# Kernel tuning notes

Measured on AMD Instinct MI355X. Metric: run time of the kernel, lower is better.

Reference implementation:

```python
import jax, jax.numpy as jnp
import numpy as np

HEADS = 16
KV_HEADS = 4
HEAD_DIM = 64
EMBED = 1024


def setup_inputs() -> dict:
    key = jax.random.key(0)
    k1, k2, k3, k4, k5 = jax.random.split(key, 5)
    B, S, G, E = 1, 2048, 2, EMBED
    scale = 1.0 / np.sqrt(E)
    x = jax.random.normal(k1, (B, S, G, E), dtype=jnp.float32)
    Wq = jax.random.normal(k2, (E, HEADS * HEAD_DIM), dtype=jnp.float32) * scale
    Wk = jax.random.normal(k3, (E, KV_HEADS * HEAD_DIM), dtype=jnp.float32) * scale
    Wv = jax.random.normal(k4, (E, KV_HEADS * HEAD_DIM), dtype=jnp.float32) * scale
    Wo = jax.random.normal(k5, (E, E), dtype=jnp.float32) * scale
    return {"x": x, "Wq": Wq, "Wk": Wk, "Wv": Wv, "Wo": Wo}


def reference(x, Wq, Wk, Wv, Wo):
    B, S, G, E = x.shape
    ratio = HEADS // KV_HEADS
    # projections over last dim (no bias, no activation)
    q = (x @ Wq).reshape(B, S, G, HEADS, HEAD_DIM)
    k = (x @ Wk).reshape(B, S, G, KV_HEADS, HEAD_DIM)
    v = (x @ Wv).reshape(B, S, G, KV_HEADS, HEAD_DIM)
    # GQA repeat_kv: each kv head repeated `ratio` times consecutively
    k = jnp.repeat(k, ratio, axis=3)  # [B,S,G,H,D]
    v = jnp.repeat(v, ratio, axis=3)
    # energy: [B,G,H,Q,K]
    energy = jnp.einsum('bqghd,bkghd->bghqk', q, k)
    # causal mask: triu(1) set to -inf (before the sqrt scaling, as in source)
    causal = jnp.triu(jnp.ones((S, S), dtype=bool), 1)
    energy = jnp.where(causal, -jnp.inf, energy)
    scores = jax.nn.softmax(energy / np.sqrt(HEAD_DIM), axis=-1)
    attn = jnp.einsum('bghqv,bvghd->bqghd', scores, v)
    attn = attn.reshape(B, S, G, E)
    return attn @ Wo
```

## Files before the change

kernel.cpp:

```cpp
#include <hip/hip_runtime.h>
#include <cstdint>
#include <cstddef>

typedef __bf16 bf16_t;
typedef bf16_t bf16x8 __attribute__((ext_vector_type(8)));
typedef float f32x4 __attribute__((ext_vector_type(4)));

__device__ inline bf16x8 load8(const float* p) {
  f32x4 a = *reinterpret_cast<const f32x4*>(p);
  f32x4 b = *reinterpret_cast<const f32x4*>(p + 4);
  bf16x8 r;
  r[0] = (bf16_t)a[0]; r[1] = (bf16_t)a[1];
  r[2] = (bf16_t)a[2]; r[3] = (bf16_t)a[3];
  r[4] = (bf16_t)b[0]; r[5] = (bf16_t)b[1];
  r[6] = (bf16_t)b[2]; r[7] = (bf16_t)b[3];
  return r;
}
__device__ inline bf16x8 load8(const bf16_t* p) {
  return *reinterpret_cast<const bf16x8*>(p);
}

__global__ __launch_bounds__(256) void cvt1_k(
    const float* __restrict__ x, const float* __restrict__ Wq,
    const float* __restrict__ Wk, const float* __restrict__ Wv,
    bf16_t* __restrict__ xb, bf16_t* __restrict__ wqb,
    bf16_t* __restrict__ wkb, bf16_t* __restrict__ wvb) {
  const int b = blockIdx.x;
  const float* s;
  bf16_t* d;
  size_t off;
  if (b < 2048) { s = x; d = xb; off = (size_t)b * 2048; }
  else if (b < 2560) { s = Wq; d = wqb; off = (size_t)(b - 2048) * 2048; }
  else if (b < 2688) { s = Wk; d = wkb; off = (size_t)(b - 2560) * 2048; }
  else { s = Wv; d = wvb; off = (size_t)(b - 2688) * 2048; }
  const size_t i = off + (size_t)threadIdx.x * 8;
  *reinterpret_cast<bf16x8*>(d + i) = load8(s + i);
}

__global__ __launch_bounds__(256) void cvt2_k(const float* __restrict__ Wo,
                                              bf16_t* __restrict__ wob) {
  const size_t i = (size_t)blockIdx.x * 2048 + (size_t)threadIdx.x * 8;
  *reinterpret_cast<bf16x8*>(wob + i) = load8(Wo + i);
}

template <typename OutT>
__device__ inline void gemm128_body(const bf16_t* __restrict__ A,
                                    const bf16_t* __restrict__ B,
                                    OutT* __restrict__ C, int m0, int K,
                                    int BN, int bn0, int CN, int cn0,
                                    float alpha) {
  __shared__ __align__(16) bf16_t As[128][40];
  __shared__ __align__(16) bf16_t Bs[128][40];

  const int tid = threadIdx.x;
  const int wave = tid >> 6, lane = tid & 63;
  const int quad = lane >> 4, l16 = lane & 15;
  const int moff = (wave & 1) * 64, noff = (wave >> 1) * 64;

  f32x4 acc[4][4];
#pragma unroll
  for (int mt = 0; mt < 4; ++mt)
#pragma unroll
    for (int nt = 0; nt < 4; ++nt) acc[mt][nt] = {0.f, 0.f, 0.f, 0.f};

  const int arow = tid >> 1, ak0 = (tid & 1) * 16;
  const int bkr = tid & 31, bnc = (tid >> 5) * 16;

  bf16x8 a0, a1, b0, b1;
  {
    const bf16_t* ap = &A[(size_t)(m0 + arow) * K + ak0];
    a0 = load8(ap); a1 = load8(ap + 8);
    const bf16_t* bp = &B[(size_t)bkr * BN + bn0 + bnc];
    b0 = load8(bp); b1 = load8(bp + 8);
  }

  for (int k0 = 0; k0 < K; k0 += 32) {
    *reinterpret_cast<bf16x8*>(&As[arow][ak0]) = a0;
    *reinterpret_cast<bf16x8*>(&As[arow][ak0 + 8]) = a1;
#pragma unroll
    for (int j = 0; j < 8; ++j) {
      Bs[bnc + j][bkr] = b0[j];
      Bs[bnc + 8 + j][bkr] = b1[j];
    }
    __syncthreads();
    if (k0 + 32 < K) {
      const bf16_t* ap = &A[(size_t)(m0 + arow) * K + k0 + 32 + ak0];
      a0 = load8(ap); a1 = load8(ap + 8);
      const bf16_t* bp = &B[(size_t)(k0 + 32 + bkr) * BN + bn0 + bnc];
      b0 = load8(bp); b1 = load8(bp + 8);
    }
    bf16x8 af[4], bfr[4];
#pragma unroll
    for (int mt = 0; mt < 4; ++mt)
      af[mt] =
          *reinterpret_cast<const bf16x8*>(&As[moff + mt * 16 + l16][quad * 8]);
#pragma unroll
    for (int nt = 0; nt < 4; ++nt)
      bfr[nt] =
          *reinterpret_cast<const bf16x8*>(&Bs[noff + nt * 16 + l16][quad * 8]);
#pragma unroll
    for (int mt = 0; mt < 4; ++mt)
#pragma unroll
      for (int nt = 0; nt < 4; ++nt)
        acc[mt][nt] = __builtin_amdgcn_mfma_f32_16x16x32_bf16(
            af[mt], bfr[nt], acc[mt][nt], 0, 0, 0);
    __syncthreads();
  }

#pragma unroll
  for (int mt = 0; mt < 4; ++mt) {
    const int crow = m0 + moff + mt * 16 + quad * 4;
#pragma unroll
    for (int nt = 0; nt < 4; ++nt) {
      const int ccol = cn0 + noff + nt * 16 + l16;
#pragma unroll
      for (int r = 0; r < 4; ++r)
        C[(size_t)(crow + r) * CN + ccol] = (OutT)(acc[mt][nt][r] * alpha);
    }
  }
}

__global__ __launch_bounds__(256, 3) void qkv_k(
    const bf16_t* __restrict__ x, const bf16_t* __restrict__ Wq,
    const bf16_t* __restrict__ Wk, const bf16_t* __restrict__ Wv,
    bf16_t* __restrict__ Qo, bf16_t* __restrict__ Ko, bf16_t* __restrict__ Vo) {
  const int n0 = blockIdx.x * 128;
  const int m0 = blockIdx.y * 128;
  const bf16_t* B;
  bf16_t* C;
  int BN, bn0;
  float alpha;
  if (n0 < 1024) {
    B = Wq; C = Qo; BN = 1024; bn0 = n0; alpha = 0.125f;
  } else if (n0 < 1280) {
    B = Wk; C = Ko; BN = 256; bn0 = n0 - 1024; alpha = 1.0f;
  } else {
    B = Wv; C = Vo; BN = 256; bn0 = n0 - 1280; alpha = 1.0f;
  }
  gemm128_body<bf16_t>(x, B, C, m0, 1024, BN, bn0, BN, bn0, alpha);
}

template <typename OutT>
__global__ __launch_bounds__(256, 3) void gemm128_k(
    const bf16_t* __restrict__ A, const bf16_t* __restrict__ B,
    OutT* __restrict__ C, int K, int N, float alpha) {
  gemm128_body<OutT>(A, B, C, blockIdx.y * 128, K, N, blockIdx.x * 128, N,
                     blockIdx.x * 128, alpha);
}

__global__ __launch_bounds__(256) void transpose_v_k(
    const bf16_t* __restrict__ V, bf16_t* __restrict__ VT) {
  __shared__ bf16_t Vs[64][72];
  const int tid = threadIdx.x;
  const int kt0 = blockIdx.x * 64;
  const int ghk = blockIdx.y;
  const int g = ghk >> 2, kh = ghk & 3;
#pragma unroll
  for (int i = 0; i < 2; ++i) {
    const int c = tid + 256 * i;
    const int row = c >> 3, d0 = (c & 7) * 8;
    *reinterpret_cast<bf16x8*>(&Vs[row][d0]) = *reinterpret_cast<const bf16x8*>(
        &V[((size_t)(kt0 + row) * 2 + g) * 256 + kh * 64 + d0]);
  }
  __syncthreads();
#pragma unroll
  for (int i = 0; i < 2; ++i) {
    const int c = tid + 256 * i;
    const int d = c >> 3, k0 = (c & 7) * 8;
    bf16x8 v;
#pragma unroll
    for (int j = 0; j < 8; ++j) v[j] = Vs[k0 + j][d];
    *reinterpret_cast<bf16x8*>(&VT[((size_t)ghk * 64 + d) * 2048 + kt0 + k0]) =
        v;
  }
}

__global__ __launch_bounds__(128, 2) void flash5_k(
    const bf16_t* __restrict__ Q, const bf16_t* __restrict__ K,
    const bf16_t* __restrict__ VT, bf16_t* __restrict__ ATTN) {
  __shared__ __align__(16) bf16_t Ks[64][64];
  __shared__ __align__(16) bf16_t Vs[64][64];
  __shared__ __align__(16) bf16_t Ps[2][32][64];

  const int tid = threadIdx.x;
  const int w = tid >> 6, lane = tid & 63;
  const int quad = lane >> 4, l16 = lane & 15;
  const int b = blockIdx.x;
  const int T = (b & 1) ? (31 - (b >> 1)) : (b >> 1);
  const int gh = blockIdx.y;
  const int g = gh >> 4, h = gh & 15, kh = h >> 2;
  const int qbase = T * 64 + w * 32;
  const int swz = ((l16 >> 2) & 3) << 4;
  const int rsw = l16 & 7;

  bf16x8 qf[2][2];
#pragma unroll
  for (int rg = 0; rg < 2; ++rg)
#pragma unroll
    for (int t = 0; t < 2; ++t)
      qf[rg][t] = *reinterpret_cast<const bf16x8*>(
          &Q[((size_t)(qbase + rg * 16 + l16) * 2 + g) * 1024 + h * 64 +
             t * 32 + quad * 8]);

  f32x4 O[2][4];
  f32x4 lp[2];
#pragma unroll
  for (int rg = 0; rg < 2; ++rg) {
    lp[rg] = {0.f, 0.f, 0.f, 0.f};
#pragma unroll
    for (int d = 0; d < 4; ++d) O[rg][d] = {0.f, 0.f, 0.f, 0.f};
  }

  bf16x8 kr[4], vr[4];
#pragma unroll
  for (int i = 0; i < 4; ++i) {
    const int c = tid + 128 * i;
    const int row = c >> 3, e0 = (c & 7) * 8;
    kr[i] = *reinterpret_cast<const bf16x8*>(
        &K[((size_t)(row)*2 + g) * 256 + kh * 64 + e0]);
    vr[i] = *reinterpret_cast<const bf16x8*>(
        &VT[((size_t)(g * 4 + kh) * 64 + row) * 2048 + e0]);
  }

  for (int kt = 0; kt <= T; ++kt) {
#pragma unroll
    for (int i = 0; i < 4; ++i) {
      const int c = tid + 128 * i;
      const int row = c >> 3;
      const int pb = (((c & 7) ^ (row & 7)) << 3);
      *reinterpret_cast<bf16x8*>(&Ks[row][pb]) = kr[i];
      *reinterpret_cast<bf16x8*>(&Vs[row][pb]) = vr[i];
    }
    __syncthreads();
    if (kt < T) {
      const int nt0 = (kt + 1) * 64;
#pragma unroll
      for (int i = 0; i < 4; ++i) {
        const int c = tid + 128 * i;
        const int row = c >> 3, e0 = (c & 7) * 8;
        kr[i] = *reinterpret_cast<const bf16x8*>(
            &K[((size_t)(nt0 + row) * 2 + g) * 256 + kh * 64 + e0]);
        vr[i] = *reinterpret_cast<const bf16x8*>(
            &VT[((size_t)(g * 4 + kh) * 64 + row) * 2048 + nt0 + e0]);
      }
    }

    f32x4 s[2][4];
#pragma unroll
    for (int nt = 0; nt < 4; ++nt) {
      bf16x8 kf0 = *reinterpret_cast<const bf16x8*>(
          &Ks[nt * 16 + l16][(quad ^ rsw) << 3]);
      bf16x8 kf1 = *reinterpret_cast<const bf16x8*>(
          &Ks[nt * 16 + l16][((4 + quad) ^ rsw) << 3]);
#pragma unroll
      for (int rg = 0; rg < 2; ++rg) {
        f32x4 z = {0.f, 0.f, 0.f, 0.f};
        z = __builtin_amdgcn_mfma_f32_16x16x32_bf16(qf[rg][0], kf0, z, 0, 0, 0);
        s[rg][nt] =
            __builtin_amdgcn_mfma_f32_16x16x32_bf16(qf[rg][1], kf1, z, 0, 0, 0);
      }
    }
    const bool diag = (kt == T);
#pragma unroll
    for (int rg = 0; rg < 2; ++rg) {
#pragma unroll
      for (int nt = 0; nt < 4; ++nt) {
        const int key = nt * 16 + l16;
#pragma unroll
        for (int r = 0; r < 4; ++r) {
          float p = __expf(s[rg][nt][r]);
          if (diag && key > w * 32 + rg * 16 + quad * 4 + r) p = 0.f;
          lp[rg][r] += p;
          Ps[w][rg * 16 + quad * 4 + r][((nt ^ quad) << 4) + l16] = (bf16_t)p;
        }
      }
    }
    bf16x8 pf[2][2];
#pragma unroll
    for (int rg = 0; rg < 2; ++rg)
#pragma unroll
      for (int t = 0; t < 2; ++t)
        pf[rg][t] = *reinterpret_cast<const bf16x8*>(
            &Ps[w][rg * 16 + l16][(t * 32 + quad * 8) ^ swz]);
#pragma unroll
    for (int dnt = 0; dnt < 4; ++dnt) {
      bf16x8 vf0 = *reinterpret_cast<const bf16x8*>(
          &Vs[dnt * 16 + l16][(quad ^ rsw) << 3]);
      bf16x8 vf1 = *reinterpret_cast<const bf16x8*>(
          &Vs[dnt * 16 + l16][((4 + quad) ^ rsw) << 3]);
#pragma unroll
      for (int rg = 0; rg < 2; ++rg) {
        O[rg][dnt] = __builtin_amdgcn_mfma_f32_16x16x32_bf16(
            pf[rg][0], vf0, O[rg][dnt], 0, 0, 0);
        O[rg][dnt] = __builtin_amdgcn_mfma_f32_16x16x32_bf16(
            pf[rg][1], vf1, O[rg][dnt], 0, 0, 0);
      }
    }
    __syncthreads();
  }

#pragma unroll
  for (int rg = 0; rg < 2; ++rg) {
#pragma unroll
    for (int off = 1; off < 16; off <<= 1)
#pragma unroll
      for (int r = 0; r < 4; ++r) lp[rg][r] += __shfl_xor(lp[rg][r], off, 64);
#pragma unroll
    for (int r = 0; r < 4; ++r) {
      const float inv = 1.f / lp[rg][r];
      const int row = qbase + rg * 16 + quad * 4 + r;
#pragma unroll
      for (int dnt = 0; dnt < 4; ++dnt)
        ATTN[((size_t)row * 2 + g) * 1024 + h * 64 + dnt * 16 + l16] =
            (bf16_t)(O[rg][dnt][r] * inv);
    }
  }
}

extern "C" void kernel_launch(void* const* d_in, const int* in_sizes, int n_in,
                              void* d_out, int out_size, void* d_ws,
                              size_t ws_size, hipStream_t stream) {
  (void)in_sizes;
  (void)n_in;
  (void)out_size;
  (void)ws_size;

  const float* x = (const float*)d_in[0];
  const float* Wq = (const float*)d_in[1];
  const float* Wk = (const float*)d_in[2];
  const float* Wv = (const float*)d_in[3];
  const float* Wo = (const float*)d_in[4];
  float* out = (float*)d_out;

  const size_t MB = 1024 * 1024;
  char* ob = (char*)d_out;
  bf16_t* Qtmp = (bf16_t*)ob;
  bf16_t* VTws = (bf16_t*)(ob + 8 * MB);
  bf16_t* wqb = (bf16_t*)(ob + 10 * MB);
  bf16_t* wkb = (bf16_t*)(ob + 12 * MB);
  bf16_t* wvb = (bf16_t*)(ob + 12 * MB + 512 * 1024);
  char* wb = (char*)d_ws;
  bf16_t* Kws = (bf16_t*)wb;
  bf16_t* Vws = (bf16_t*)(wb + 2 * MB);
  bf16_t* ATTNws = (bf16_t*)(wb + 4 * MB);
  bf16_t* xb = ATTNws;
  bf16_t* wob = Kws;

  cvt1_k<<<dim3(2816), dim3(256), 0, stream>>>(x, Wq, Wk, Wv, xb, wqb, wkb,
                                               wvb);
  qkv_k<<<dim3(12, 32), dim3(256), 0, stream>>>(xb, wqb, wkb, wvb, Qtmp, Kws,
                                                Vws);
  transpose_v_k<<<dim3(32, 8), dim3(256), 0, stream>>>(Vws, VTws);
  flash5_k<<<dim3(32, 32), dim3(128), 0, stream>>>(Qtmp, Kws, VTws, ATTNws);
  cvt2_k<<<dim3(512), dim3(256), 0, stream>>>(Wo, wob);
  gemm128_k<float><<<dim3(8, 32), dim3(256), 0, stream>>>(ATTNws, wob, out,
                                                          1024, 1024, 1.0f);
}
```

Baseline: 198.8 us.

## Pre-transpose weights to N-major bf16 and reorder flash tile scheduling

Weights are now converted to bf16 and transposed once, in a tiled shared-memory kernel, so the GEMM B-operand loads become contiguous 16-byte rows written to LDS with vector stores instead of scalar transposed stores. The separate Wo conversion is merged into the weight-transpose kernel, and buffers are relocated to fit. The flash kernel's causal tile ordering changes from alternating pairs to groups of eight in a zigzag pattern for load balance. The cost is an extra transpose pass over the weights.

```diff
diff --git a/kernel.cpp b/kernel.cpp
--- a/kernel.cpp
+++ b/kernel.cpp
@@ -20,35 +20,54 @@
   return *reinterpret_cast<const bf16x8*>(p);
 }
 
-__global__ __launch_bounds__(256) void cvt1_k(
-    const float* __restrict__ x, const float* __restrict__ Wq,
-    const float* __restrict__ Wk, const float* __restrict__ Wv,
-    bf16_t* __restrict__ xb, bf16_t* __restrict__ wqb,
-    bf16_t* __restrict__ wkb, bf16_t* __restrict__ wvb) {
+__global__ __launch_bounds__(256) void cvtx_k(const float* __restrict__ x,
+                                              bf16_t* __restrict__ xb) {
+  const size_t i = (size_t)blockIdx.x * 2048 + (size_t)threadIdx.x * 8;
+  *reinterpret_cast<bf16x8*>(xb + i) = load8(x + i);
+}
+
+__global__ __launch_bounds__(256) void cvtT_k(
+    const float* __restrict__ Wq, const float* __restrict__ Wk,
+    const float* __restrict__ Wv, const float* __restrict__ Wo,
+    bf16_t* __restrict__ wqT, bf16_t* __restrict__ wkT,
+    bf16_t* __restrict__ wvT, bf16_t* __restrict__ woT) {
+  __shared__ bf16_t Ts[64][72];
   const int b = blockIdx.x;
-  const float* s;
-  bf16_t* d;
-  size_t off;
-  if (b < 2048) { s = x; d = xb; off = (size_t)b * 2048; }
-  else if (b < 2560) { s = Wq; d = wqb; off = (size_t)(b - 2048) * 2048; }
-  else if (b < 2688) { s = Wk; d = wkb; off = (size_t)(b - 2560) * 2048; }
-  else { s = Wv; d = wvb; off = (size_t)(b - 2688) * 2048; }
-  const size_t i = off + (size_t)threadIdx.x * 8;
-  *reinterpret_cast<bf16x8*>(d + i) = load8(s + i);
-}
-
-__global__ __launch_bounds__(256) void cvt2_k(const float* __restrict__ Wo,
-                                              bf16_t* __restrict__ wob) {
-  const size_t i = (size_t)blockIdx.x * 2048 + (size_t)threadIdx.x * 8;
-  *reinterpret_cast<bf16x8*>(wob + i) = load8(Wo + i);
+  const float* S;
+  bf16_t* D;
+  int N, idx;
+  if (b < 256) { S = Wq; D = wqT; N = 1024; idx = b; }
+  else if (b < 320) { S = Wk; D = wkT; N = 256; idx = b - 256; }
+  else if (b < 384) { S = Wv; D = wvT; N = 256; idx = b - 320; }
+  else { S = Wo; D = woT; N = 1024; idx = b - 384; }
+  const int ntl = (N == 1024) ? 4 : 2;
+  const int kt0 = (idx >> ntl) * 64;
+  const int n0 = (idx & ((1 << ntl) - 1)) * 64;
+  const int tid = threadIdx.x;
+#pragma unroll
+  for (int i = 0; i < 2; ++i) {
+    const int c = tid + 256 * i;
+    const int row = c >> 3, col0 = (c & 7) * 8;
+    *reinterpret_cast<bf16x8*>(&Ts[row][col0]) =
+        load8(&S[(size_t)(kt0 + row) * N + n0 + col0]);
+  }
+  __syncthreads();
+#pragma unroll
+  for (int i = 0; i < 2; ++i) {
+    const int c = tid + 256 * i;
+    const int nrow = c >> 3, k0 = (c & 7) * 8;
+    bf16x8 v;
+#pragma unroll
+    for (int j = 0; j < 8; ++j) v[j] = Ts[k0 + j][nrow];
+    *reinterpret_cast<bf16x8*>(&D[(size_t)(n0 + nrow) * 1024 + kt0 + k0]) = v;
+  }
 }
 
 template <typename OutT>
-__device__ inline void gemm128_body(const bf16_t* __restrict__ A,
-                                    const bf16_t* __restrict__ B,
-                                    OutT* __restrict__ C, int m0, int K,
-                                    int BN, int bn0, int CN, int cn0,
-                                    float alpha) {
+__device__ inline void gemm_bt_body(const bf16_t* __restrict__ A,
+                                    const bf16_t* __restrict__ BT,
+                                    OutT* __restrict__ C, int m0, int bt0,
+                                    int K, int CN, int cn0, float alpha) {
   __shared__ __align__(16) bf16_t As[128][40];
   __shared__ __align__(16) bf16_t Bs[128][40];
 
@@ -64,29 +83,25 @@
     for (int nt = 0; nt < 4; ++nt) acc[mt][nt] = {0.f, 0.f, 0.f, 0.f};
 
   const int arow = tid >> 1, ak0 = (tid & 1) * 16;
-  const int bkr = tid & 31, bnc = (tid >> 5) * 16;
 
   bf16x8 a0, a1, b0, b1;
   {
     const bf16_t* ap = &A[(size_t)(m0 + arow) * K + ak0];
     a0 = load8(ap); a1 = load8(ap + 8);
-    const bf16_t* bp = &B[(size_t)bkr * BN + bn0 + bnc];
+    const bf16_t* bp = &BT[(size_t)(bt0 + arow) * K + ak0];
     b0 = load8(bp); b1 = load8(bp + 8);
   }
 
   for (int k0 = 0; k0 < K; k0 += 32) {
     *reinterpret_cast<bf16x8*>(&As[arow][ak0]) = a0;
     *reinterpret_cast<bf16x8*>(&As[arow][ak0 + 8]) = a1;
-#pragma unroll
-    for (int j = 0; j < 8; ++j) {
-      Bs[bnc + j][bkr] = b0[j];
-      Bs[bnc + 8 + j][bkr] = b1[j];
-    }
+    *reinterpret_cast<bf16x8*>(&Bs[arow][ak0]) = b0;
+    *reinterpret_cast<bf16x8*>(&Bs[arow][ak0 + 8]) = b1;
     __syncthreads();
     if (k0 + 32 < K) {
       const bf16_t* ap = &A[(size_t)(m0 + arow) * K + k0 + 32 + ak0];
       a0 = load8(ap); a1 = load8(ap + 8);
-      const bf16_t* bp = &B[(size_t)(k0 + 32 + bkr) * BN + bn0 + bnc];
+      const bf16_t* bp = &BT[(size_t)(bt0 + arow) * K + k0 + 32 + ak0];
       b0 = load8(bp); b1 = load8(bp + 8);
     }
     bf16x8 af[4], bfr[4];
@@ -121,30 +136,30 @@
 }
 
 __global__ __launch_bounds__(256, 3) void qkv_k(
-    const bf16_t* __restrict__ x, const bf16_t* __restrict__ Wq,
-    const bf16_t* __restrict__ Wk, const bf16_t* __restrict__ Wv,
+    const bf16_t* __restrict__ x, const bf16_t* __restrict__ wqT,
+    const bf16_t* __restrict__ wkT, const bf16_t* __restrict__ wvT,
     bf16_t* __restrict__ Qo, bf16_t* __restrict__ Ko, bf16_t* __restrict__ Vo) {
   const int n0 = blockIdx.x * 128;
   const int m0 = blockIdx.y * 128;
-  const bf16_t* B;
+  const bf16_t* BT;
   bf16_t* C;
-  int BN, bn0;
+  int CN, bn0;
   float alpha;
   if (n0 < 1024) {
-    B = Wq; C = Qo; BN = 1024; bn0 = n0; alpha = 0.125f;
+    BT = wqT; C = Qo; CN = 1024; bn0 = n0; alpha = 0.125f;
   } else if (n0 < 1280) {
-    B = Wk; C = Ko; BN = 256; bn0 = n0 - 1024; alpha = 1.0f;
+    BT = wkT; C = Ko; CN = 256; bn0 = n0 - 1024; alpha = 1.0f;
   } else {
-    B = Wv; C = Vo; BN = 256; bn0 = n0 - 1280; alpha = 1.0f;
-  }
-  gemm128_body<bf16_t>(x, B, C, m0, 1024, BN, bn0, BN, bn0, alpha);
+    BT = wvT; C = Vo; CN = 256; bn0 = n0 - 1280; alpha = 1.0f;
+  }
+  gemm_bt_body<bf16_t>(x, BT, C, m0, bn0, 1024, CN, bn0, alpha);
 }
 
 template <typename OutT>
-__global__ __launch_bounds__(256, 3) void gemm128_k(
-    const bf16_t* __restrict__ A, const bf16_t* __restrict__ B,
+__global__ __launch_bounds__(256, 3) void gemm_bt_k(
+    const bf16_t* __restrict__ A, const bf16_t* __restrict__ BT,
     OutT* __restrict__ C, int K, int N, float alpha) {
-  gemm128_body<OutT>(A, B, C, blockIdx.y * 128, K, N, blockIdx.x * 128, N,
+  gemm_bt_body<OutT>(A, BT, C, blockIdx.y * 128, blockIdx.x * 128, K, N,
                      blockIdx.x * 128, alpha);
 }
 
@@ -175,7 +190,7 @@
   }
 }
 
-__global__ __launch_bounds__(128, 2) void flash5_k(
+__global__ __launch_bounds__(128, 2) void flash6_k(
     const bf16_t* __restrict__ Q, const bf16_t* __restrict__ K,
     const bf16_t* __restrict__ VT, bf16_t* __restrict__ ATTN) {
   __shared__ __align__(16) bf16_t Ks[64][64];
@@ -186,7 +201,11 @@
   const int w = tid >> 6, lane = tid & 63;
   const int quad = lane >> 4, l16 = lane & 15;
   const int b = blockIdx.x;
-  const int T = (b & 1) ? (31 - (b >> 1)) : (b >> 1);
+  const int j8 = b & 7, i8 = b >> 3;
+  const int T = (i8 == 0) ? j8
+              : (i8 == 1) ? (15 - j8)
+              : (i8 == 2) ? (16 + j8)
+                          : (31 - j8);
   const int gh = blockIdx.y;
   const int g = gh >> 4, h = gh & 15, kh = h >> 2;
   const int qbase = T * 64 + w * 32;
@@ -336,23 +355,23 @@
   char* ob = (char*)d_out;
   bf16_t* Qtmp = (bf16_t*)ob;
   bf16_t* VTws = (bf16_t*)(ob + 8 * MB);
-  bf16_t* wqb = (bf16_t*)(ob + 10 * MB);
-  bf16_t* wkb = (bf16_t*)(ob + 12 * MB);
-  bf16_t* wvb = (bf16_t*)(ob + 12 * MB + 512 * 1024);
+  bf16_t* wqT = (bf16_t*)(ob + 10 * MB);
+  bf16_t* wkT = (bf16_t*)(ob + 12 * MB);
+  bf16_t* wvT = (bf16_t*)(ob + 12 * MB + 512 * 1024);
+  bf16_t* Vws = (bf16_t*)(ob + 13 * MB);
   char* wb = (char*)d_ws;
   bf16_t* Kws = (bf16_t*)wb;
-  bf16_t* Vws = (bf16_t*)(wb + 2 * MB);
+  bf16_t* woT = (bf16_t*)(wb + 2 * MB);
   bf16_t* ATTNws = (bf16_t*)(wb + 4 * MB);
   bf16_t* xb = ATTNws;
-  bf16_t* wob = Kws;
-
-  cvt1_k<<<dim3(2816), dim3(256), 0, stream>>>(x, Wq, Wk, Wv, xb, wqb, wkb,
-                                               wvb);
-  qkv_k<<<dim3(12, 32), dim3(256), 0, stream>>>(xb, wqb, wkb, wvb, Qtmp, Kws,
+
+  cvtx_k<<<dim3(2048), dim3(256), 0, stream>>>(x, xb);
+  cvtT_k<<<dim3(640), dim3(256), 0, stream>>>(Wq, Wk, Wv, Wo, wqT, wkT, wvT,
+                                              woT);
+  qkv_k<<<dim3(12, 32), dim3(256), 0, stream>>>(xb, wqT, wkT, wvT, Qtmp, Kws,
                                                 Vws);
   transpose_v_k<<<dim3(32, 8), dim3(256), 0, stream>>>(Vws, VTws);
-  flash5_k<<<dim3(32, 32), dim3(128), 0, stream>>>(Qtmp, Kws, VTws, ATTNws);
-  cvt2_k<<<dim3(512), dim3(256), 0, stream>>>(Wo, wob);
-  gemm128_k<float><<<dim3(8, 32), dim3(256), 0, stream>>>(ATTNws, wob, out,
+  flash6_k<<<dim3(32, 32), dim3(128), 0, stream>>>(Qtmp, Kws, VTws, ATTNws);
+  gemm_bt_k<float><<<dim3(8, 32), dim3(256), 0, stream>>>(ATTNws, woT, out,
                                                           1024, 1024, 1.0f);
 }
```

Measured after the change: 188.0 us. -5.4%, faster.
